# Kernel tuning notes

Hardware: AMD Instinct MI355X
Metric: run time of the kernel (lower is better)

Reference implementation:

```python
import jax, jax.numpy as jnp
import numpy as np

N_NODES = 50000
N_EDGES = 800000
FEAT = 256
HID = 64
OUT = 40


def setup_inputs() -> dict:
    key = jax.random.key(0)
    ks = jax.random.split(key, 5)
    x = jax.random.normal(ks[0], (N_NODES, FEAT), dtype=jnp.float32)
    edge_index = jax.random.randint(ks[1], (2, N_EDGES), 0, N_NODES, dtype=jnp.int64)
    # Glorot-style init for GCN linear weights
    W1 = jax.random.normal(ks[2], (FEAT, HID), dtype=jnp.float32) * (1.0 / np.sqrt(FEAT))
    b1 = jnp.zeros((HID,), dtype=jnp.float32)
    W2 = jax.random.normal(ks[3], (HID, OUT), dtype=jnp.float32) * (1.0 / np.sqrt(HID))
    b2 = jnp.zeros((OUT,), dtype=jnp.float32)
    return {"x": x, "edge_index": edge_index, "W1": W1, "b1": b1, "W2": W2, "b2": b2}


def _gcn_conv(h, W, b, src, dst, norm, n_nodes):
    # GCNConv: linear transform first (reduces message width), then
    # symmetric-normalized gather-scale-scatter aggregation.
    h = h @ W  # [N, out]
    msg = h[src] * norm[:, None]  # [E+N, out] gather + scale
    agg = jax.ops.segment_sum(msg, dst, num_segments=n_nodes)  # scatter-add
    return agg + b


def reference(x, edge_index, W1, b1, W2, b2):
    n = x.shape[0]
    # add self loops (GCNConv default add_self_loops=True)
    loops = jnp.arange(n, dtype=edge_index.dtype)
    src = jnp.concatenate([edge_index[0], loops])
    dst = jnp.concatenate([edge_index[1], loops])
    # symmetric normalization: deg computed on A + I (in-degree at dst)
    deg = jax.ops.segment_sum(jnp.ones_like(dst, dtype=x.dtype), dst, num_segments=n)
    dinv = jax.lax.rsqrt(deg)  # deg >= 1 due to self loops
    norm = dinv[src] * dinv[dst]  # [E+N]

    h = jax.nn.relu(_gcn_conv(x, W1, b1, src, dst, norm, n))
    # dropout is identity in eval mode (reference baseline)
    h = _gcn_conv(h, W2, b2, src, dst, norm, n)
    return jax.nn.log_softmax(h, axis=1)
```

## Files before the change

kernel.cpp:

```cpp
#include <hip/hip_runtime.h>
#include <hip/hip_bf16.h>


constexpr int NN   = 50000;
constexpr int NNP  = 50048;
constexpr int ZR   = 50000;
constexpr int NE   = 800000;
constexpr int FEAT = 256;
constexpr int HID  = 64;
constexpr int OUTD = 40;
constexpr int NC   = (NN + 255) / 256;
constexpr int FCH  = 2048;
constexpr int NCH  = (NE + FCH - 1) / FCH;

typedef short bf16x8 __attribute__((ext_vector_type(8)));
typedef float f32x4  __attribute__((ext_vector_type(4)));

__device__ __forceinline__ float b2f(__hip_bfloat16 v) { return __bfloat162float(v); }
__device__ __forceinline__ float bflo(unsigned u) { return __uint_as_float(u << 16); }
__device__ __forceinline__ float bfhi(unsigned u) { return __uint_as_float(u & 0xffff0000u); }
__device__ __forceinline__ unsigned short f2bu(float f) {
    __hip_bfloat16 h = __float2bfloat16(f);
    return *(unsigned short*)&h;
}
__device__ __forceinline__ unsigned pack2bf(float a, float b) {
    return (unsigned)f2bu(a) | ((unsigned)f2bu(b) << 16);
}
__device__ __forceinline__ float loadF(const void* p, int i, bool f32) {
    return f32 ? ((const float*)p)[i] : b2f(((const __hip_bfloat16*)p)[i]);
}
__device__ __forceinline__ int loadE(const int* ei, int e, int row, bool i64) {
    long long idx = (long long)row * NE + e;
    return i64 ? ei[2 * idx] : ei[idx];
}
__device__ __forceinline__ bf16x8 pack8(float4 a, float4 b) {
    bf16x8 r;
    r[0] = (short)f2bu(a.x); r[1] = (short)f2bu(a.y);
    r[2] = (short)f2bu(a.z); r[3] = (short)f2bu(a.w);
    r[4] = (short)f2bu(b.x); r[5] = (short)f2bu(b.y);
    r[6] = (short)f2bu(b.z); r[7] = (short)f2bu(b.w);
    return r;
}

__global__ __launch_bounds__(256) void k_zero(const unsigned* __restrict__ xw,
                                              const int* __restrict__ ew,
                                              int* flags, int* cnt,
                                              unsigned* __restrict__ h2pad) {
    int i = blockIdx.x * 256 + threadIdx.x;
    if (i < NN) cnt[i] = 0;
    if (blockIdx.x == 0 && threadIdx.x < 20) h2pad[threadIdx.x] = 0;
    if (blockIdx.x == 0 && threadIdx.x == 0) {
        int outliers = 0;
        for (int k = 0; k < 256; k++) {
            int e = (xw[k] >> 7) & 0xFF;
            if (e < 100 || e > 140) outliers++;
        }
        flags[0] = (outliers > 64) ? 1 : 0;
        int nz = 0;
        for (int k = 1; k < 64; k += 2)
            if (ew[k] != 0) nz++;
        flags[1] = (nz == 0) ? 1 : 0;
    }
}

__global__ __launch_bounds__(256) void k_hist(const int* __restrict__ ei,
                                              const int* __restrict__ flags,
                                              int* cnt, int* __restrict__ rank) {
    const bool i64 = flags[1] != 0;
    int e = blockIdx.x * 256 + threadIdx.x;
    if (e < NE) rank[e] = atomicAdd(&cnt[loadE(ei, e, 1, i64)], 1);
}
__global__ __launch_bounds__(256) void k_scan1(const int* __restrict__ cnt,
                                               int* row_start, int* partial, float* dinv) {
    __shared__ int s[256];
    int t = threadIdx.x, i = blockIdx.x * 256 + t;
    int v = (i < NN) ? cnt[i] : 0;
    if (i < NN) dinv[i] = rsqrtf(1.0f + (float)v);
    s[t] = v;
    __syncthreads();
    for (int off = 1; off < 256; off <<= 1) {
        int tmp = (t >= off) ? s[t - off] : 0;
        __syncthreads();
        s[t] += tmp;
        __syncthreads();
    }
    if (i < NN) row_start[i] = s[t] - v;
    if (t == 255) partial[blockIdx.x] = s[255];
}
__global__ __launch_bounds__(256) void k_scan2p(const int* __restrict__ partial, int* pp) {
    __shared__ int s[256];
    int t = threadIdx.x;
    int v = (t < NC) ? partial[t] : 0;
    s[t] = v;
    __syncthreads();
    for (int off = 1; off < 256; off <<= 1) {
        int tmp = (t >= off) ? s[t - off] : 0;
        __syncthreads();
        s[t] += tmp;
        __syncthreads();
    }
    pp[t] = s[t] - v;
}
__global__ __launch_bounds__(256) void k_fill(const int* __restrict__ ei,
                                              const int* __restrict__ flags,
                                              const int* __restrict__ row_start,
                                              const int* __restrict__ pp,
                                              const int* __restrict__ rank,
                                              unsigned short* __restrict__ csr16) {
    const bool i64 = flags[1] != 0;
    const int cls = blockIdx.x & 7;
    const int e0 = (blockIdx.x >> 3) * FCH;
#pragma unroll
    for (int k = 0; k < FCH / 256; k++) {
        int e = e0 + k * 256 + threadIdx.x;
        if (e < NE) {
            int d = loadE(ei, e, 1, i64);
            if (d / 6250 == cls) {
                int s = loadE(ei, e, 0, i64);
                csr16[row_start[d] + pp[d >> 8] + rank[e]] = (unsigned short)s;
            }
        }
    }
}

__global__ __launch_bounds__(256) void k_gemm1(const void* __restrict__ xb,
                                               const void* __restrict__ W1,
                                               const float* __restrict__ dinv,
                                               const int* __restrict__ flags,
                                               unsigned short* __restrict__ h1u) {
    __shared__ __align__(16) unsigned short wt16[64 * 264];
    const bool f32 = flags[0] != 0;
    const int t = threadIdx.x;
    if (f32) {
        const float* wf = (const float*)W1;
        for (int i = t * 4; i < FEAT * HID; i += 1024) {
            float4 w = *(const float4*)(wf + i);
            int k = i >> 6, n0 = i & 63;
            wt16[(n0 + 0) * 264 + k] = f2bu(w.x);
            wt16[(n0 + 1) * 264 + k] = f2bu(w.y);
            wt16[(n0 + 2) * 264 + k] = f2bu(w.z);
            wt16[(n0 + 3) * 264 + k] = f2bu(w.w);
        }
    } else {
        const unsigned short* wu = (const unsigned short*)W1;
        for (int i = t * 4; i < FEAT * HID; i += 1024) {
            ushort4 w = *(const ushort4*)(wu + i);
            int k = i >> 6, n0 = i & 63;
            wt16[(n0 + 0) * 264 + k] = w.x;
            wt16[(n0 + 1) * 264 + k] = w.y;
            wt16[(n0 + 2) * 264 + k] = w.z;
            wt16[(n0 + 3) * 264 + k] = w.w;
        }
    }
    const int wv = t >> 6, lane = t & 63, l15 = lane & 15, quad = lane >> 4;
    const int gr = blockIdx.x * 64 + wv * 16 + l15;
    const bool rowok = gr < NN;
    f32x4 acc[4];
#pragma unroll
    for (int nt = 0; nt < 4; nt++) acc[nt] = (f32x4){0.f, 0.f, 0.f, 0.f};
    __syncthreads();

    if (f32) {
        const float* xr = (const float*)xb + (size_t)gr * FEAT + quad * 8;
        float4 z4 = make_float4(0, 0, 0, 0);
        float4 c0 = rowok ? *(const float4*)xr : z4;
        float4 c1 = rowok ? *(const float4*)(xr + 4) : z4;
#pragma unroll
        for (int ks = 0; ks < 8; ks++) {
            float4 n0 = z4, n1 = z4;
            if (ks < 7 && rowok) {
                n0 = *(const float4*)(xr + (ks + 1) * 32);
                n1 = *(const float4*)(xr + (ks + 1) * 32 + 4);
            }
            bf16x8 a = pack8(c0, c1);
            const unsigned short* wk = wt16 + ks * 32 + quad * 8;
#pragma unroll
            for (int nt = 0; nt < 4; nt++) {
                bf16x8 b = *(const bf16x8*)(wk + (size_t)(nt * 16 + l15) * 264);
                acc[nt] = __builtin_amdgcn_mfma_f32_16x16x32_bf16(a, b, acc[nt], 0, 0, 0);
            }
            c0 = n0; c1 = n1;
        }
    } else {
        const unsigned short* xr = (const unsigned short*)xb + (size_t)gr * FEAT + quad * 8;
        bf16x8 zz = (bf16x8){0, 0, 0, 0, 0, 0, 0, 0};
        bf16x8 cur = rowok ? *(const bf16x8*)xr : zz;
#pragma unroll
        for (int ks = 0; ks < 8; ks++) {
            bf16x8 nxt = zz;
            if (ks < 7 && rowok) nxt = *(const bf16x8*)(xr + (ks + 1) * 32);
            const unsigned short* wk = wt16 + ks * 32 + quad * 8;
#pragma unroll
            for (int nt = 0; nt < 4; nt++) {
                bf16x8 b = *(const bf16x8*)(wk + (size_t)(nt * 16 + l15) * 264);
                acc[nt] = __builtin_amdgcn_mfma_f32_16x16x32_bf16(cur, b, acc[nt], 0, 0, 0);
            }
            cur = nxt;
        }
    }
    const int rbase = blockIdx.x * 64 + wv * 16 + quad * 4;
    float dv[4];
#pragma unroll
    for (int r = 0; r < 4; r++) dv[r] = (rbase + r < NN) ? dinv[rbase + r] : 0.f;
#pragma unroll
    for (int r = 0; r < 4; r++) {
        int grow = rbase + r;
#pragma unroll
        for (int nt = 0; nt < 4; nt++)
            h1u[(size_t)grow * HID + nt * 16 + l15] = f2bu(acc[nt][r] * dv[r]);
    }
}

__global__ __launch_bounds__(256, 4) void k_gather1f(const uint2* __restrict__ h1v,
                                                  const float* __restrict__ dinv,
                                                  const int* __restrict__ row_start,
                                                  const int* __restrict__ pp,
                                                  const int* __restrict__ cnt,
                                                  const unsigned short* __restrict__ csr16,
                                                  const void* __restrict__ W2,
                                                  const void* __restrict__ b1,
                                                  const int* __restrict__ flags,
                                                  unsigned short* __restrict__ h2u) {
    __shared__ __align__(16) float w2t[OUTD * 68];
    __shared__ __align__(16) float gbuf[16 * 68];
    __shared__ float dns[16];
    const bool f32 = flags[0] != 0;
    const int t = threadIdx.x;
    for (int i = t; i < HID * OUTD; i += 256) {
        int c = i >> 6, k = i & 63;
        w2t[c * 68 + k] = loadF(W2, (size_t)k * OUTD + c, f32);
    }
    const int nl = t >> 4, l16 = t & 15;
    const int n = blockIdx.x * 16 + nl;
    const float dn = dinv[n];
    uint2 u0 = h1v[n * 16 + l16];
    float a0 = bflo(u0.x), a1 = bfhi(u0.x), a2 = bflo(u0.y), a3 = bfhi(u0.y);
    float e0 = 0.f, e1 = 0.f, e2 = 0.f, e3 = 0.f;
    const int rs = row_start[n] + pp[n >> 8], c = cnt[n];
    for (int base = 0; base < c; base += 16) {
        int rem = c - base;
        int sv = (l16 < rem) ? (int)csr16[rs + base + l16] : ZR;
        int s0  = __shfl(sv, 0, 16),  s1  = __shfl(sv, 1, 16);
        int s2  = __shfl(sv, 2, 16),  s3  = __shfl(sv, 3, 16);
        int s4  = __shfl(sv, 4, 16),  s5  = __shfl(sv, 5, 16);
        int s6  = __shfl(sv, 6, 16),  s7  = __shfl(sv, 7, 16);
        int s8  = __shfl(sv, 8, 16),  s9  = __shfl(sv, 9, 16);
        int s10 = __shfl(sv, 10, 16), s11 = __shfl(sv, 11, 16);
        int s12 = __shfl(sv, 12, 16), s13 = __shfl(sv, 13, 16);
        int s14 = __shfl(sv, 14, 16), s15 = __shfl(sv, 15, 16);
        uint2 b0  = h1v[(s0  << 4) | l16], b1v_ = h1v[(s1  << 4) | l16];
        uint2 b2_ = h1v[(s2  << 4) | l16], b3_ = h1v[(s3  << 4) | l16];
        uint2 b4_ = h1v[(s4  << 4) | l16], b5_ = h1v[(s5  << 4) | l16];
        uint2 b6_ = h1v[(s6  << 4) | l16], b7_ = h1v[(s7  << 4) | l16];
        uint2 d0  = h1v[(s8  << 4) | l16], d1  = h1v[(s9  << 4) | l16];
        uint2 d2  = h1v[(s10 << 4) | l16], d3  = h1v[(s11 << 4) | l16];
        uint2 d4  = h1v[(s12 << 4) | l16], d5  = h1v[(s13 << 4) | l16];
        uint2 d6  = h1v[(s14 << 4) | l16], d7  = h1v[(s15 << 4) | l16];
        __builtin_amdgcn_sched_barrier(0);
        a0 += bflo(b0.x);  a1 += bfhi(b0.x);  a2 += bflo(b0.y);  a3 += bfhi(b0.y);
        a0 += bflo(b1v_.x); a1 += bfhi(b1v_.x); a2 += bflo(b1v_.y); a3 += bfhi(b1v_.y);
        a0 += bflo(b2_.x); a1 += bfhi(b2_.x); a2 += bflo(b2_.y); a3 += bfhi(b2_.y);
        a0 += bflo(b3_.x); a1 += bfhi(b3_.x); a2 += bflo(b3_.y); a3 += bfhi(b3_.y);
        a0 += bflo(b4_.x); a1 += bfhi(b4_.x); a2 += bflo(b4_.y); a3 += bfhi(b4_.y);
        a0 += bflo(b5_.x); a1 += bfhi(b5_.x); a2 += bflo(b5_.y); a3 += bfhi(b5_.y);
        a0 += bflo(b6_.x); a1 += bfhi(b6_.x); a2 += bflo(b6_.y); a3 += bfhi(b6_.y);
        a0 += bflo(b7_.x); a1 += bfhi(b7_.x); a2 += bflo(b7_.y); a3 += bfhi(b7_.y);
        e0 += bflo(d0.x);  e1 += bfhi(d0.x);  e2 += bflo(d0.y);  e3 += bfhi(d0.y);
        e0 += bflo(d1.x);  e1 += bfhi(d1.x);  e2 += bflo(d1.y);  e3 += bfhi(d1.y);
        e0 += bflo(d2.x);  e1 += bfhi(d2.x);  e2 += bflo(d2.y);  e3 += bfhi(d2.y);
        e0 += bflo(d3.x);  e1 += bfhi(d3.x);  e2 += bflo(d3.y);  e3 += bfhi(d3.y);
        e0 += bflo(d4.x);  e1 += bfhi(d4.x);  e2 += bflo(d4.y);  e3 += bfhi(d4.y);
        e0 += bflo(d5.x);  e1 += bfhi(d5.x);  e2 += bflo(d5.y);  e3 += bfhi(d5.y);
        e0 += bflo(d6.x);  e1 += bfhi(d6.x);  e2 += bflo(d6.y);  e3 += bfhi(d6.y);
        e0 += bflo(d7.x);  e1 += bfhi(d7.x);  e2 += bflo(d7.y);  e3 += bfhi(d7.y);
    }
    int cb = 4 * l16;
    float g0 = fmaxf(dn * (a0 + e0) + loadF(b1, cb, f32), 0.f);
    float g1 = fmaxf(dn * (a1 + e1) + loadF(b1, cb + 1, f32), 0.f);
    float g2 = fmaxf(dn * (a2 + e2) + loadF(b1, cb + 2, f32), 0.f);
    float g3 = fmaxf(dn * (a3 + e3) + loadF(b1, cb + 3, f32), 0.f);
    *(float4*)(gbuf + nl * 68 + cb) = make_float4(g0, g1, g2, g3);
    if (l16 == 0) dns[nl] = dn;
    __syncthreads();
    for (int idx = t; idx < 16 * OUTD; idx += 256) {
        int node = idx / OUTD, col = idx % OUTD;
        const float4* gp = (const float4*)(gbuf + node * 68);
        const float4* wp = (const float4*)(w2t + col * 68);
        float o = 0.f;
#pragma unroll 4
        for (int k4 = 0; k4 < 16; k4++) {
            float4 a = gp[k4], b = wp[k4];
            o += a.x * b.x + a.y * b.y + a.z * b.z + a.w * b.w;
        }
        h2u[(size_t)(blockIdx.x * 16 + node) * OUTD + col] = f2bu(o * dns[node]);
    }
}

__global__ __launch_bounds__(256, 4) void k_gather2(const uint2* __restrict__ h2v,
                                                 const float* __restrict__ dinv,
                                                 const int* __restrict__ row_start,
                                                 const int* __restrict__ pp,
                                                 const int* __restrict__ cnt,
                                                 const unsigned short* __restrict__ csr16,
                                                 const void* __restrict__ b2,
                                                 const int* __restrict__ flags,
                                                 void* __restrict__ out) {
    const bool f32 = flags[0] != 0;
    const int t = threadIdx.x;
    const int nl = t >> 4, l16 = t & 15;
    const int n = blockIdx.x * 16 + nl;
    const bool act = l16 < 10;
    const float dn = dinv[n];
    const int lclamp = act ? l16 : 9;
    uint2 u0 = h2v[n * 10 + lclamp];
    float a0 = bflo(u0.x), a1 = bfhi(u0.x), a2 = bflo(u0.y), a3 = bfhi(u0.y);
    float e0 = 0.f, e1 = 0.f, e2 = 0.f, e3 = 0.f;
    const int rs = row_start[n] + pp[n >> 8], c = cnt[n];
    for (int base = 0; base < c; base += 16) {
        int rem = c - base;
        int sv = (l16 < rem) ? (int)csr16[rs + base + l16] : ZR;
        int s0  = __shfl(sv, 0, 16),  s1  = __shfl(sv, 1, 16);
        int s2  = __shfl(sv, 2, 16),  s3  = __shfl(sv, 3, 16);
        int s4  = __shfl(sv, 4, 16),  s5  = __shfl(sv, 5, 16);
        int s6  = __shfl(sv, 6, 16),  s7  = __shfl(sv, 7, 16);
        int s8  = __shfl(sv, 8, 16),  s9  = __shfl(sv, 9, 16);
        int s10 = __shfl(sv, 10, 16), s11 = __shfl(sv, 11, 16);
        int s12 = __shfl(sv, 12, 16), s13 = __shfl(sv, 13, 16);
        int s14 = __shfl(sv, 14, 16), s15 = __shfl(sv, 15, 16);
        uint2 b0  = h2v[s0  * 10 + lclamp], b1_ = h2v[s1  * 10 + lclamp];
        uint2 b2_ = h2v[s2  * 10 + lclamp], b3_ = h2v[s3  * 10 + lclamp];
        uint2 b4_ = h2v[s4  * 10 + lclamp], b5_ = h2v[s5  * 10 + lclamp];
        uint2 b6_ = h2v[s6  * 10 + lclamp], b7_ = h2v[s7  * 10 + lclamp];
        uint2 d0  = h2v[s8  * 10 + lclamp], d1  = h2v[s9  * 10 + lclamp];
        uint2 d2  = h2v[s10 * 10 + lclamp], d3  = h2v[s11 * 10 + lclamp];
        uint2 d4  = h2v[s12 * 10 + lclamp], d5  = h2v[s13 * 10 + lclamp];
        uint2 d6  = h2v[s14 * 10 + lclamp], d7  = h2v[s15 * 10 + lclamp];
        __builtin_amdgcn_sched_barrier(0);
        a0 += bflo(b0.x);  a1 += bfhi(b0.x);  a2 += bflo(b0.y);  a3 += bfhi(b0.y);
        a0 += bflo(b1_.x); a1 += bfhi(b1_.x); a2 += bflo(b1_.y); a3 += bfhi(b1_.y);
        a0 += bflo(b2_.x); a1 += bfhi(b2_.x); a2 += bflo(b2_.y); a3 += bfhi(b2_.y);
        a0 += bflo(b3_.x); a1 += bfhi(b3_.x); a2 += bflo(b3_.y); a3 += bfhi(b3_.y);
        a0 += bflo(b4_.x); a1 += bfhi(b4_.x); a2 += bflo(b4_.y); a3 += bfhi(b4_.y);
        a0 += bflo(b5_.x); a1 += bfhi(b5_.x); a2 += bflo(b5_.y); a3 += bfhi(b5_.y);
        a0 += bflo(b6_.x); a1 += bfhi(b6_.x); a2 += bflo(b6_.y); a3 += bfhi(b6_.y);
        a0 += bflo(b7_.x); a1 += bfhi(b7_.x); a2 += bflo(b7_.y); a3 += bfhi(b7_.y);
        e0 += bflo(d0.x);  e1 += bfhi(d0.x);  e2 += bflo(d0.y);  e3 += bfhi(d0.y);
        e0 += bflo(d1.x);  e1 += bfhi(d1.x);  e2 += bflo(d1.y);  e3 += bfhi(d1.y);
        e0 += bflo(d2.x);  e1 += bfhi(d2.x);  e2 += bflo(d2.y);  e3 += bfhi(d2.y);
        e0 += bflo(d3.x);  e1 += bfhi(d3.x);  e2 += bflo(d3.y);  e3 += bfhi(d3.y);
        e0 += bflo(d4.x);  e1 += bfhi(d4.x);  e2 += bflo(d4.y);  e3 += bfhi(d4.y);
        e0 += bflo(d5.x);  e1 += bfhi(d5.x);  e2 += bflo(d5.y);  e3 += bfhi(d5.y);
        e0 += bflo(d6.x);  e1 += bfhi(d6.x);  e2 += bflo(d6.y);  e3 += bfhi(d6.y);
        e0 += bflo(d7.x);  e1 += bfhi(d7.x);  e2 += bflo(d7.y);  e3 += bfhi(d7.y);
    }
    int cb = 4 * l16;
    float v0 = -3.0e38f, v1 = -3.0e38f, v2 = -3.0e38f, v3 = -3.0e38f;
    if (act) {
        v0 = dn * (a0 + e0) + loadF(b2, cb, f32);
        v1 = dn * (a1 + e1) + loadF(b2, cb + 1, f32);
        v2 = dn * (a2 + e2) + loadF(b2, cb + 2, f32);
        v3 = dn * (a3 + e3) + loadF(b2, cb + 3, f32);
    }
    float mx = fmaxf(fmaxf(v0, v1), fmaxf(v2, v3));
#pragma unroll
    for (int off = 8; off; off >>= 1) mx = fmaxf(mx, __shfl_xor(mx, off, 16));
    float ev = act ? expf(v0 - mx) + expf(v1 - mx) + expf(v2 - mx) + expf(v3 - mx) : 0.f;
#pragma unroll
    for (int off = 8; off; off >>= 1) ev += __shfl_xor(ev, off, 16);
    float lg = logf(ev);
    if (act) {
        float r0 = v0 - mx - lg, r1 = v1 - mx - lg;
        float r2 = v2 - mx - lg, r3 = v3 - mx - lg;
        if (f32) {
            *(float4*)((float*)out + (size_t)n * OUTD + cb) = make_float4(r0, r1, r2, r3);
        } else {
            ((uint2*)out)[(size_t)n * 10 + l16] = make_uint2(pack2bf(r0, r1), pack2bf(r2, r3));
        }
    }
}

extern "C" void kernel_launch(void* const* d_in, const int* in_sizes, int n_in,
                              void* d_out, int out_size, void* d_ws, size_t ws_size,
                              hipStream_t stream) {
    const void* x  = d_in[0];
    const int*  ei = (const int*)d_in[1];
    const void* W1 = d_in[2];
    const void* b1 = d_in[3];
    const void* W2 = d_in[4];
    const void* b2 = d_in[5];

    float* ws        = (float*)d_ws;
    int*   flags     = (int*)ws;
    float* dinv      = ws + 16;
    int*   cnt       = (int*)(dinv + 50048);
    int*   row_start = cnt + 50048;
    int*   partial   = row_start + 50048;
    int*   pp        = partial + 256;
    int*   rank      = pp + 256;
    unsigned short* csr16 = (unsigned short*)(rank + NE);
    unsigned short* h1u   = csr16 + NE;
    unsigned short* h2u   = h1u + (size_t)NNP * HID;
    unsigned* h2pad = (unsigned*)(h2u + (size_t)ZR * OUTD);

    k_zero  <<<(NN + 255) / 256, 256, 0, stream>>>((const unsigned*)x, ei, flags, cnt, h2pad);
    k_hist  <<<(NE + 255) / 256, 256, 0, stream>>>(ei, flags, cnt, rank);
    k_scan1 <<<NC, 256, 0, stream>>>(cnt, row_start, partial, dinv);
    k_scan2p<<<1, 256, 0, stream>>>(partial, pp);
    k_fill  <<<NCH * 8, 256, 0, stream>>>(ei, flags, row_start, pp, rank, csr16);
    k_gemm1 <<<NNP / 64, 256, 0, stream>>>(x, W1, dinv, flags, h1u);
    k_gather1f<<<NN / 16, 256, 0, stream>>>((const uint2*)h1u, dinv, row_start, pp, cnt, csr16,
                                            W2, b1, flags, h2u);
    k_gather2<<<NN / 16, 256, 0, stream>>>((const uint2*)h2u, dinv, row_start, pp, cnt, csr16,
                                           b2, flags, d_out);
}
```

Measured before the change: 234.3 us.

## Stage layer-1 neighbor gathers through LDS via global_load_lds in gather kernel

Replaces the per-lane register gather of neighbor rows in k_gather1f with wave-cooperative global_load_lds DMA into a per-wave LDS staging buffer. Each wave now loops to the maximum neighbor count of its four nodes, and every lane then reads its slice back from LDS. The aim is fewer VGPRs tied up in in-flight loads and wider, coalesced 128-byte row fetches. In exchange it adds 32KB of LDS per block, lowers the launch-bounds occupancy hint from 4 to 3, and spends idle work on waves whose nodes have uneven degrees.

```diff
diff --git a/kernel.cpp b/kernel.cpp
--- a/kernel.cpp
+++ b/kernel.cpp
@@ -40,6 +40,11 @@
     r[4] = (short)f2bu(b.x); r[5] = (short)f2bu(b.y);
     r[6] = (short)f2bu(b.z); r[7] = (short)f2bu(b.w);
     return r;
+}
+__device__ __forceinline__ void gload_lds4(const void* g, void* l) {
+    __builtin_amdgcn_global_load_lds(
+        (const __attribute__((address_space(1))) void*)g,
+        (__attribute__((address_space(3))) void*)l, 4, 0, 0);
 }
 
 __global__ __launch_bounds__(256) void k_zero(const unsigned* __restrict__ xw,
@@ -211,7 +216,7 @@
     }
 }
 
-__global__ __launch_bounds__(256, 4) void k_gather1f(const uint2* __restrict__ h1v,
+__global__ __launch_bounds__(256, 3) void k_gather1f(const uint2* __restrict__ h1v,
                                                   const float* __restrict__ dinv,
                                                   const int* __restrict__ row_start,
                                                   const int* __restrict__ pp,
@@ -221,6 +226,7 @@
                                                   const void* __restrict__ b1,
                                                   const int* __restrict__ flags,
                                                   unsigned short* __restrict__ h2u) {
+    __shared__ __align__(16) unsigned stage[4][64][32];
     __shared__ __align__(16) float w2t[OUTD * 68];
     __shared__ __align__(16) float gbuf[16 * 68];
     __shared__ float dns[16];
@@ -230,49 +236,37 @@
         int c = i >> 6, k = i & 63;
         w2t[c * 68 + k] = loadF(W2, (size_t)k * OUTD + c, f32);
     }
-    const int nl = t >> 4, l16 = t & 15;
+    const int wid = t >> 6, lane = t & 63;
+    const int q = lane >> 4, l16 = lane & 15;
+    const int hi = lane >> 5;
+    const int nl = t >> 4;
     const int n = blockIdx.x * 16 + nl;
     const float dn = dinv[n];
+    const unsigned* h1d = (const unsigned*)h1v;
     uint2 u0 = h1v[n * 16 + l16];
     float a0 = bflo(u0.x), a1 = bfhi(u0.x), a2 = bflo(u0.y), a3 = bfhi(u0.y);
     float e0 = 0.f, e1 = 0.f, e2 = 0.f, e3 = 0.f;
     const int rs = row_start[n] + pp[n >> 8], c = cnt[n];
-    for (int base = 0; base < c; base += 16) {
-        int rem = c - base;
-        int sv = (l16 < rem) ? (int)csr16[rs + base + l16] : ZR;
-        int s0  = __shfl(sv, 0, 16),  s1  = __shfl(sv, 1, 16);
-        int s2  = __shfl(sv, 2, 16),  s3  = __shfl(sv, 3, 16);
-        int s4  = __shfl(sv, 4, 16),  s5  = __shfl(sv, 5, 16);
-        int s6  = __shfl(sv, 6, 16),  s7  = __shfl(sv, 7, 16);
-        int s8  = __shfl(sv, 8, 16),  s9  = __shfl(sv, 9, 16);
-        int s10 = __shfl(sv, 10, 16), s11 = __shfl(sv, 11, 16);
-        int s12 = __shfl(sv, 12, 16), s13 = __shfl(sv, 13, 16);
-        int s14 = __shfl(sv, 14, 16), s15 = __shfl(sv, 15, 16);
-        uint2 b0  = h1v[(s0  << 4) | l16], b1v_ = h1v[(s1  << 4) | l16];
-        uint2 b2_ = h1v[(s2  << 4) | l16], b3_ = h1v[(s3  << 4) | l16];
-        uint2 b4_ = h1v[(s4  << 4) | l16], b5_ = h1v[(s5  << 4) | l16];
-        uint2 b6_ = h1v[(s6  << 4) | l16], b7_ = h1v[(s7  << 4) | l16];
-        uint2 d0  = h1v[(s8  << 4) | l16], d1  = h1v[(s9  << 4) | l16];
-        uint2 d2  = h1v[(s10 << 4) | l16], d3  = h1v[(s11 << 4) | l16];
-        uint2 d4  = h1v[(s12 << 4) | l16], d5  = h1v[(s13 << 4) | l16];
-        uint2 d6  = h1v[(s14 << 4) | l16], d7  = h1v[(s15 << 4) | l16];
+    int cmax = max(c, __shfl_xor(c, 16, 64));
+    cmax = max(cmax, __shfl_xor(cmax, 32, 64));
+    for (int base = 0; base < cmax; base += 16) {
         __builtin_amdgcn_sched_barrier(0);
-        a0 += bflo(b0.x);  a1 += bfhi(b0.x);  a2 += bflo(b0.y);  a3 += bfhi(b0.y);
-        a0 += bflo(b1v_.x); a1 += bfhi(b1v_.x); a2 += bflo(b1v_.y); a3 += bfhi(b1v_.y);
-        a0 += bflo(b2_.x); a1 += bfhi(b2_.x); a2 += bflo(b2_.y); a3 += bfhi(b2_.y);
-        a0 += bflo(b3_.x); a1 += bfhi(b3_.x); a2 += bflo(b3_.y); a3 += bfhi(b3_.y);
-        a0 += bflo(b4_.x); a1 += bfhi(b4_.x); a2 += bflo(b4_.y); a3 += bfhi(b4_.y);
-        a0 += bflo(b5_.x); a1 += bfhi(b5_.x); a2 += bflo(b5_.y); a3 += bfhi(b5_.y);
-        a0 += bflo(b6_.x); a1 += bfhi(b6_.x); a2 += bflo(b6_.y); a3 += bfhi(b6_.y);
-        a0 += bflo(b7_.x); a1 += bfhi(b7_.x); a2 += bflo(b7_.y); a3 += bfhi(b7_.y);
-        e0 += bflo(d0.x);  e1 += bfhi(d0.x);  e2 += bflo(d0.y);  e3 += bfhi(d0.y);
-        e0 += bflo(d1.x);  e1 += bfhi(d1.x);  e2 += bflo(d1.y);  e3 += bfhi(d1.y);
-        e0 += bflo(d2.x);  e1 += bfhi(d2.x);  e2 += bflo(d2.y);  e3 += bfhi(d2.y);
-        e0 += bflo(d3.x);  e1 += bfhi(d3.x);  e2 += bflo(d3.y);  e3 += bfhi(d3.y);
-        e0 += bflo(d4.x);  e1 += bfhi(d4.x);  e2 += bflo(d4.y);  e3 += bfhi(d4.y);
-        e0 += bflo(d5.x);  e1 += bfhi(d5.x);  e2 += bflo(d5.y);  e3 += bfhi(d5.y);
-        e0 += bflo(d6.x);  e1 += bfhi(d6.x);  e2 += bflo(d6.y);  e3 += bfhi(d6.y);
-        e0 += bflo(d7.x);  e1 += bfhi(d7.x);  e2 += bflo(d7.y);  e3 += bfhi(d7.y);
+        int sv = (base + l16 < c) ? (int)csr16[rs + base + l16] : ZR;
+#pragma unroll
+        for (int i = 0; i < 32; i++) {
+            int s = __shfl(sv, 2 * i + hi, 64);
+            gload_lds4(h1d + (((unsigned)s) << 5) + (lane & 31), &stage[wid][2 * i][0]);
+        }
+        asm volatile("s_waitcnt vmcnt(0)" ::: "memory");
+#pragma unroll
+        for (int j = 0; j < 16; j++) {
+            uint2 v = *(const uint2*)&stage[wid][q * 16 + j][l16 * 2];
+            if (j & 1) {
+                e0 += bflo(v.x); e1 += bfhi(v.x); e2 += bflo(v.y); e3 += bfhi(v.y);
+            } else {
+                a0 += bflo(v.x); a1 += bfhi(v.x); a2 += bflo(v.y); a3 += bfhi(v.y);
+            }
+        }
     }
     int cb = 4 * l16;
     float g0 = fmaxf(dn * (a0 + e0) + loadF(b1, cb, f32), 0.f);
```

New measurement: 246.3 us. 5.1% more time.
